# Kernel tuning notes

Measured on AMD Instinct MI355X. Metric: run time of the kernel, lower is better.

The kernel has to match this reference:

```python
import jax, jax.numpy as jnp
import numpy as np

NEG_INF = -1e10  # matches torch's -10000000000.0 fill


def setup_inputs() -> dict:
    key = jax.random.key(0)
    k1, k2, k3, k4, k5, k6 = jax.random.split(key, 6)
    B, N, D_IN, D_HID, D_OUT = 8, 2048, 512, 512, 512
    H = jax.random.normal(k1, (B, N, D_IN), dtype=jnp.float32)
    bias = jax.random.normal(k2, (B, N, N), dtype=jnp.float32)
    mask = jax.random.randint(k3, (B, N, N), 0, 2, dtype=jnp.int32)
    s = 1.0 / np.sqrt(D_IN)
    Wq = jax.random.normal(k4, (D_IN, D_HID), dtype=jnp.float32) * s
    Wk = jax.random.normal(k5, (D_IN, D_HID), dtype=jnp.float32) * s
    Wv = jax.random.normal(k6, (D_IN, D_OUT), dtype=jnp.float32) * s
    return {"H": H, "bias": bias, "mask": mask, "Wq": Wq, "Wk": Wk, "Wv": Wv}


def reference(H, bias, mask, Wq, Wk, Wv):
    # Q,K: [B,N,d_hid], V: [B,N,d_out]
    Q = H @ Wq
    K = H @ Wk
    V = H @ Wv
    d = Q.shape[-1]
    scale = 1.0 / jnp.sqrt(jnp.asarray(d, dtype=Q.dtype))
    # scores: [B,N,N]; scale, add bias, then fill masked-out entries
    scores = jnp.einsum("bnd,bmd->bnm", Q, K) * scale + bias
    scores = jnp.where(mask == 0, jnp.asarray(NEG_INF, scores.dtype), scores)
    atn = jax.nn.softmax(scores, axis=-1)
    return jnp.einsum("bnm,bmo->bno", atn, V)
```

## Files before the change

### kernel.cpp

```cpp
#include <hip/hip_runtime.h>
#include <hip/hip_bf16.h>

typedef __attribute__((ext_vector_type(8))) short short8;
typedef __attribute__((ext_vector_type(4))) float floatx4;
typedef __attribute__((ext_vector_type(4))) int intx4;
typedef __attribute__((ext_vector_type(4))) unsigned short ushortx4;

#define NB 8
#define NN 2048
#define DD 512

__device__ __forceinline__ unsigned short f2bf(float f) {
  union { float f; unsigned int u; } v; v.f = f;
  unsigned int u = v.u;
  return (unsigned short)((u + 0x7fffu + ((u >> 16) & 1u)) >> 16);
}
__device__ __forceinline__ float bf2f(unsigned short s) {
  union { unsigned int u; float f; } v; v.u = ((unsigned int)s) << 16;
  return v.f;
}

typedef __attribute__((address_space(3))) unsigned short lds_us;
typedef __attribute__((address_space(1))) const unsigned short glb_us;

__device__ __forceinline__ void ld_lds16(const unsigned short* g, unsigned short* l) {
  __builtin_amdgcn_global_load_lds((glb_us*)g, (lds_us*)l, 16, 0, 0);
}

__global__ __launch_bounds__(256) void mha_cvtH(const float* __restrict__ H,
                                                unsigned short* __restrict__ Hb, int n8) {
  int i = blockIdx.x * 256 + threadIdx.x;
  if (i >= n8) return;
  const float4* src = (const float4*)H;
  float4 a = src[2 * i], b = src[2 * i + 1];
  short8 o;
  o[0] = (short)f2bf(a.x); o[1] = (short)f2bf(a.y); o[2] = (short)f2bf(a.z); o[3] = (short)f2bf(a.w);
  o[4] = (short)f2bf(b.x); o[5] = (short)f2bf(b.y); o[6] = (short)f2bf(b.z); o[7] = (short)f2bf(b.w);
  *(short8*)(Hb + 8 * i) = o;
}

__global__ __launch_bounds__(256) void mha_prep(const floatx4* __restrict__ bias,
                                                const intx4* __restrict__ mask,
                                                ushortx4* __restrict__ bm) {
  int i = blockIdx.x * 256 + threadIdx.x;
  floatx4 bv = __builtin_nontemporal_load(&bias[i]);
  intx4 mv = __builtin_nontemporal_load(&mask[i]);
  const unsigned short NINF = 0xFF80;
  ushortx4 o;
  o.x = mv.x ? f2bf(bv.x) : NINF;
  o.y = mv.y ? f2bf(bv.y) : NINF;
  o.z = mv.z ? f2bf(bv.z) : NINF;
  o.w = mv.w ? f2bf(bv.w) : NINF;
  __builtin_nontemporal_store(o, &bm[i]);
}

__global__ __launch_bounds__(256) void mha_tW(const float* __restrict__ Wq, const float* __restrict__ Wk,
                                              const float* __restrict__ Wv,
                                              unsigned short* __restrict__ Wqt, unsigned short* __restrict__ Wkt,
                                              unsigned short* __restrict__ Wvt) {
  const float* W = (blockIdx.z == 0) ? Wq : (blockIdx.z == 1) ? Wk : Wv;
  unsigned short* Wt = (blockIdx.z == 0) ? Wqt : (blockIdx.z == 1) ? Wkt : Wvt;
  __shared__ float tile[32][33];
  int d0 = blockIdx.x * 32, k0 = blockIdx.y * 32;
  int t = threadIdx.x, r = t >> 3, c4 = (t & 7) * 4;
  float4 v = *(const float4*)(W + (size_t)(k0 + r) * DD + d0 + c4);
  tile[r][c4] = v.x; tile[r][c4 + 1] = v.y; tile[r][c4 + 2] = v.z; tile[r][c4 + 3] = v.w;
  __syncthreads();
  union { unsigned short s[4]; uint2 v; } u;
  u.s[0] = f2bf(tile[c4][r]);     u.s[1] = f2bf(tile[c4 + 1][r]);
  u.s[2] = f2bf(tile[c4 + 2][r]); u.s[3] = f2bf(tile[c4 + 3][r]);
  *(uint2*)(Wt + (size_t)(d0 + r) * DD + k0 + c4) = u.v;
}

__global__ __launch_bounds__(256) void mha_tV(const unsigned short* __restrict__ Vr,
                                              unsigned short* __restrict__ Vt) {
  int b = blockIdx.z;
  int d0 = blockIdx.x * 32, n0 = blockIdx.y * 32;
  __shared__ unsigned short tile[32][34];
  int t = threadIdx.x, r = t >> 3, c4 = (t & 7) * 4;
  union { uint2 v; unsigned short s[4]; } u;
  u.v = *(const uint2*)(Vr + ((size_t)b * NN + n0 + r) * DD + d0 + c4);
  tile[r][c4] = u.s[0]; tile[r][c4 + 1] = u.s[1]; tile[r][c4 + 2] = u.s[2]; tile[r][c4 + 3] = u.s[3];
  __syncthreads();
  union { unsigned short s[4]; uint2 v; } o;
  o.s[0] = tile[c4][r]; o.s[1] = tile[c4 + 1][r]; o.s[2] = tile[c4 + 2][r]; o.s[3] = tile[c4 + 3][r];
  *(uint2*)(Vt + ((size_t)b * DD + d0 + r) * NN + n0 + c4) = o.v;
}

__device__ __forceinline__ void stage_tile_async(const unsigned short* __restrict__ g, int ld,
                                                 unsigned short* s, int t) {
#pragma unroll
  for (int h = 0; h < 2; ++h) {
    int c = t + h * 256;
    int r = c >> 2, p = c & 3;
    int seg = (p - (r >> 1)) & 3;
    ld_lds16(g + (size_t)r * ld + seg * 8, s + c * 8);
  }
}

__device__ __forceinline__ void mfma_step(const unsigned short* As, const unsigned short* Bs,
                                          int wr, int wc, int quad, int lr, floatx4 acc[4][4]) {
  short8 a[4], b[4];
#pragma unroll
  for (int i = 0; i < 4; ++i) {
    int ra = wr * 64 + i * 16 + lr;
    int rb = wc * 64 + i * 16 + lr;
    a[i] = *(const short8*)(As + ra * 32 + ((quad + (ra >> 1)) & 3) * 8);
    b[i] = *(const short8*)(Bs + rb * 32 + ((quad + (rb >> 1)) & 3) * 8);
  }
#pragma unroll
  for (int i = 0; i < 4; ++i)
#pragma unroll
    for (int j = 0; j < 4; ++j)
      acc[i][j] = __builtin_amdgcn_mfma_f32_16x16x32_bf16(a[i], b[j], acc[i][j], 0, 0, 0);
}

__global__ __launch_bounds__(256) void mha_proj(const unsigned short* __restrict__ Hb,
                                                const unsigned short* __restrict__ Wqt,
                                                const unsigned short* __restrict__ Wkt,
                                                const unsigned short* __restrict__ Wvt,
                                                unsigned short* __restrict__ Qb,
                                                unsigned short* __restrict__ Kb,
                                                unsigned short* __restrict__ Vr) {
  const unsigned short* Wt = (blockIdx.z == 0) ? Wqt : (blockIdx.z == 1) ? Wkt : Wvt;
  unsigned short* dst = (blockIdx.z == 0) ? Qb : (blockIdx.z == 1) ? Kb : Vr;
  __shared__ unsigned short As[128 * 32], Bs[128 * 32];
  int t = threadIdx.x, wave = t >> 6, lane = t & 63, quad = lane >> 4, lr = lane & 15;
  int wr = wave >> 1, wc = wave & 1;
  int m0 = blockIdx.y * 128, n0 = blockIdx.x * 128;
  floatx4 acc[4][4] = {};
  for (int k0 = 0; k0 < DD; k0 += 32) {
    __syncthreads();
    stage_tile_async(Hb + (size_t)m0 * DD + k0, DD, As, t);
    stage_tile_async(Wt + (size_t)n0 * DD + k0, DD, Bs, t);
    __syncthreads();
    mfma_step(As, Bs, wr, wc, quad, lr, acc);
  }
#pragma unroll
  for (int i = 0; i < 4; ++i)
#pragma unroll
    for (int j = 0; j < 4; ++j)
#pragma unroll
      for (int r = 0; r < 4; ++r) {
        int row = m0 + wr * 64 + i * 16 + quad * 4 + r;
        int col = n0 + wc * 64 + j * 16 + lr;
        dst[(size_t)row * DD + col] = f2bf(acc[i][j][r]);
      }
}

__global__ __launch_bounds__(512) void mha_attn(const unsigned short* __restrict__ Qb,
                                                const unsigned short* __restrict__ Kb,
                                                const unsigned short* __restrict__ Vtb,
                                                const unsigned short* __restrict__ bmE,
                                                float* __restrict__ out) {
  __shared__ unsigned short KV[2][16384];
  __shared__ unsigned short Ps[64 * 128];
  __shared__ unsigned short Bm[64 * 128];
  __shared__ float ls[64];

  const int b = blockIdx.x;
  const int i0 = blockIdx.y * 64;
  const int t = threadIdx.x;
  const int wave = t >> 6, lane = t & 63, quad = lane >> 4, lr = lane & 15;
  const int wi = wave & 3;
  const int wj = wave >> 2;
  const float scale = 0.04419417382415922f;

  const unsigned short* Q = Qb + (size_t)b * NN * DD;
  const unsigned short* K = Kb + (size_t)b * NN * DD;
  const unsigned short* V = Vtb + (size_t)b * DD * NN;
  const unsigned short* bm = bmE + (size_t)b * NN * NN;

  if (t < 64) ls[t] = 0.0f;

  short8 q[16];
#pragma unroll
  for (int kc = 0; kc < 16; ++kc)
    q[kc] = *(const short8*)(Q + (size_t)(i0 + wi * 16 + lr) * DD + kc * 32 + quad * 8);

  floatx4 acc_o[4][4] = {};
  float rs[4] = {0.f, 0.f, 0.f, 0.f};

  const int krow = t >> 2, kphys = t & 3;
  const int kseg = (kphys - (krow >> 1)) & 3;

#pragma unroll
  for (int h = 0; h < 4; ++h)
    ld_lds16(K + (size_t)krow * DD + h * 32 + kseg * 8, KV[0] + h * 4096 + t * 8);
#pragma unroll
  for (int h = 0; h < 2; ++h) {
    int c = t + h * 512, row = c >> 4, phys = c & 15, seg = (phys - row) & 15;
    ld_lds16(bm + (size_t)(i0 + row) * NN + seg * 8, Bm + c * 8);
  }
  __syncthreads();

  for (int tt = 0; tt < 16; ++tt) {
    const int j0 = tt * 128;
    floatx4 acc_s[4] = {};

#pragma unroll
    for (int s = 0; s < 4; ++s) {
      if (s < 3) {
#pragma unroll
        for (int h = 0; h < 4; ++h)
          ld_lds16(K + (size_t)(j0 + krow) * DD + (s + 1) * 128 + h * 32 + kseg * 8,
                   KV[(s + 1) & 1] + h * 4096 + t * 8);
      } else {
#pragma unroll
        for (int h = 0; h < 4; ++h) {
          int c = t + h * 512, row = c >> 2, phys = c & 3, seg = (phys - (row >> 1)) & 3;
          ld_lds16(V + (size_t)row * NN + j0 + seg * 8, KV[0] + c * 8);
        }
      }
      const unsigned short* Ks = KV[s & 1];
#pragma unroll
      for (int kc = 0; kc < 4; ++kc) {
#pragma unroll
        for (int jt = 0; jt < 4; ++jt) {
          int rb = wj * 64 + jt * 16 + lr;
          short8 bf = *(const short8*)(Ks + kc * 4096 + rb * 32 + ((quad + (rb >> 1)) & 3) * 8);
          acc_s[jt] = __builtin_amdgcn_mfma_f32_16x16x32_bf16(q[s * 4 + kc], bf, acc_s[jt], 0, 0, 0);
        }
      }
      if (s == 3) {
#pragma unroll
        for (int jt = 0; jt < 4; ++jt) {
          int col = wj * 64 + jt * 16 + lr;
#pragma unroll
          for (int rr = 0; rr < 4; ++rr) {
            int row = wi * 16 + quad * 4 + rr;
            float bi = bf2f(Bm[row * 128 + ((((col >> 3) + row) & 15) << 3) + (col & 7)]);
            float e = __expf(acc_s[jt][rr] * scale + bi - 16.0f);
            unsigned short eb = f2bf(e);
            rs[rr] += bf2f(eb);
            Ps[row * 128 + (col ^ ((row & 7) << 3))] = eb;
          }
        }
      }
      __syncthreads();
    }

#pragma unroll
    for (int jc = 0; jc < 4; ++jc) {
      if (jc < 3) {
#pragma unroll
        for (int h = 0; h < 4; ++h) {
          int c = t + h * 512, row = c >> 2, phys = c & 3, seg = (phys - (row >> 1)) & 3;
          ld_lds16(V + (size_t)row * NN + j0 + (jc + 1) * 32 + seg * 8, KV[(jc + 1) & 1] + c * 8);
        }
      } else if (tt < 15) {
#pragma unroll
        for (int h = 0; h < 4; ++h)
          ld_lds16(K + (size_t)(j0 + 128 + krow) * DD + h * 32 + kseg * 8,
                   KV[0] + h * 4096 + t * 8);
#pragma unroll
        for (int h = 0; h < 2; ++h) {
          int c = t + h * 512, row = c >> 4, phys = c & 15, seg = (phys - row) & 15;
          ld_lds16(bm + (size_t)(i0 + row) * NN + j0 + 128 + seg * 8, Bm + c * 8);
        }
      }
      const unsigned short* Vs = KV[jc & 1];
      short8 pa[4];
#pragma unroll
      for (int it = 0; it < 4; ++it)
        pa[it] = *(const short8*)(Ps + (it * 16 + lr) * 128 +
                                  ((jc * 32 + quad * 8) ^ ((lr & 7) << 3)));
#pragma unroll
      for (int dt = 0; dt < 4; ++dt) {
        int rb = wave * 64 + dt * 16 + lr;
        short8 bf = *(const short8*)(Vs + rb * 32 + ((quad + (rb >> 1)) & 3) * 8);
#pragma unroll
        for (int it = 0; it < 4; ++it)
          acc_o[it][dt] = __builtin_amdgcn_mfma_f32_16x16x32_bf16(pa[it], bf, acc_o[it][dt], 0, 0, 0);
      }
      __syncthreads();
    }
  }

#pragma unroll
  for (int rr = 0; rr < 4; ++rr) {
    float v = rs[rr];
    v += __shfl_xor(v, 1);
    v += __shfl_xor(v, 2);
    v += __shfl_xor(v, 4);
    v += __shfl_xor(v, 8);
    if (lr == 0) atomicAdd(&ls[wi * 16 + quad * 4 + rr], v);
  }
  __syncthreads();

  float* ob = out + ((size_t)b * NN + i0) * DD;
#pragma unroll
  for (int it = 0; it < 4; ++it)
#pragma unroll
    for (int rr = 0; rr < 4; ++rr) {
      int row = it * 16 + quad * 4 + rr;
      float linv = 1.0f / ls[row];
#pragma unroll
      for (int dt = 0; dt < 4; ++dt)
        __builtin_nontemporal_store(acc_o[it][dt][rr] * linv,
                                    &ob[(size_t)row * DD + wave * 64 + dt * 16 + lr]);
    }
}

extern "C" void kernel_launch(void* const* d_in, const int* in_sizes, int n_in,
                              void* d_out, int out_size, void* d_ws, size_t ws_size,
                              hipStream_t stream) {
  const float* H = (const float*)d_in[0];
  const float* bias = (const float*)d_in[1];
  const int* mask = (const int*)d_in[2];
  const float* Wq = (const float*)d_in[3];
  const float* Wk = (const float*)d_in[4];
  const float* Wv = (const float*)d_in[5];
  float* out = (float*)d_out;
  char* ws = (char*)d_ws;

  const size_t SZ_QKV = (size_t)NB * NN * DD * 2;
  const size_t SZ_W = (size_t)DD * DD * 2;
  unsigned short* Qb = (unsigned short*)(ws);
  unsigned short* Kb = (unsigned short*)(ws + SZ_QKV);
  unsigned short* Vt = (unsigned short*)(ws + 2 * SZ_QKV);
  char* base2 = ws + 3 * SZ_QKV;
  unsigned short* bmE = (unsigned short*)(base2);
  unsigned short* Hb = (unsigned short*)(base2);
  unsigned short* Wqt = (unsigned short*)(base2 + SZ_QKV);
  unsigned short* Wkt = (unsigned short*)(base2 + SZ_QKV + SZ_W);
  unsigned short* Wvt = (unsigned short*)(base2 + SZ_QKV + 2 * SZ_W);
  unsigned short* Vr = (unsigned short*)(base2 + SZ_QKV + 3 * SZ_W);

  mha_cvtH<<<dim3((NB * NN * DD / 8) / 256), 256, 0, stream>>>(H, Hb, NB * NN * DD / 8);
  mha_tW<<<dim3(DD / 32, DD / 32, 3), 256, 0, stream>>>(Wq, Wk, Wv, Wqt, Wkt, Wvt);
  mha_proj<<<dim3(DD / 128, NB * NN / 128, 3), 256, 0, stream>>>(Hb, Wqt, Wkt, Wvt, Qb, Kb, Vr);
  mha_tV<<<dim3(DD / 32, NN / 32, NB), 256, 0, stream>>>(Vr, Vt);
  mha_prep<<<dim3((NB * NN * NN / 4) / 256), 256, 0, stream>>>((const floatx4*)bias,
                                                               (const intx4*)mask, (ushortx4*)bmE);
  mha_attn<<<dim3(NB, NN / 64), 512, 0, stream>>>(Qb, Kb, Vt, bmE, out);
}
```

Measured before the change: 471.8 us.

## Triple-buffer K/V LDS staging with fine-grained vmcnt waits and MFMA priority

Replaces the double-buffered K/V LDS ring, which was guarded by full __syncthreads, with a three-slot rotating buffer. Each stage now waits only on partial vmcnt counts followed by a bare s_barrier, so two global-to-LDS loads can stay in flight while MFMAs run. The MFMA loops are wrapped in s_setprio to favour compute issue, and the row-sum scratch reuses the Ps buffer to offset the extra LDS. The risks are added LDS per block (a third 32KB slot), which may lower occupancy, and correctness depending on hand-counted waitcnt values. The final iteration also prefetches a wrapped-around tile that is never used.

```diff
diff --git a/kernel.cpp b/kernel.cpp
--- a/kernel.cpp
+++ b/kernel.cpp
@@ -9,6 +9,11 @@
 #define NB 8
 #define NN 2048
 #define DD 512
+
+#define WAITV(N) asm volatile("s_waitcnt vmcnt(" #N ")" ::: "memory")
+#define WAITLK() asm volatile("s_waitcnt lgkmcnt(0)" ::: "memory")
+#define BAR() __builtin_amdgcn_s_barrier()
+#define CLOB() asm volatile("" ::: "memory")
 
 __device__ __forceinline__ unsigned short f2bf(float f) {
   union { float f; unsigned int u; } v; v.f = f;
@@ -148,15 +153,76 @@
       }
 }
 
+
+__device__ __forceinline__ void stageK(const unsigned short* __restrict__ K, int j0, int kblk,
+                                       unsigned short* buf, int krow, int kseg, int t) {
+#pragma unroll
+  for (int h = 0; h < 4; ++h)
+    ld_lds16(K + (size_t)(j0 + krow) * DD + kblk * 128 + h * 32 + kseg * 8,
+             buf + h * 4096 + t * 8);
+}
+
+__device__ __forceinline__ void stageV(const unsigned short* __restrict__ V, int j0, int jc,
+                                       unsigned short* buf, int t) {
+#pragma unroll
+  for (int h = 0; h < 4; ++h) {
+    int c = t + h * 512, row = c >> 2, phys = c & 3, seg = (phys - (row >> 1)) & 3;
+    ld_lds16(V + (size_t)row * NN + j0 + jc * 32 + seg * 8, buf + c * 8);
+  }
+}
+
+__device__ __forceinline__ void stageBm(const unsigned short* __restrict__ bm, int i0, int j0,
+                                        unsigned short* Bm, int t) {
+#pragma unroll
+  for (int h = 0; h < 2; ++h) {
+    int c = t + h * 512, row = c >> 4, phys = c & 15, seg = (phys - row) & 15;
+    ld_lds16(bm + (size_t)(i0 + row) * NN + j0 + seg * 8, Bm + c * 8);
+  }
+}
+
+template <int SQ>
+__device__ __forceinline__ void qk_stage(const unsigned short* Ks, const short8* q,
+                                         int wj, int quad, int lr, floatx4 (&acc_s)[4]) {
+  __builtin_amdgcn_s_setprio(1);
+#pragma unroll
+  for (int kc = 0; kc < 4; ++kc) {
+#pragma unroll
+    for (int jt = 0; jt < 4; ++jt) {
+      int rb = wj * 64 + jt * 16 + lr;
+      short8 bf = *(const short8*)(Ks + kc * 4096 + rb * 32 + ((quad + (rb >> 1)) & 3) * 8);
+      acc_s[jt] = __builtin_amdgcn_mfma_f32_16x16x32_bf16(q[SQ * 4 + kc], bf, acc_s[jt], 0, 0, 0);
+    }
+  }
+  __builtin_amdgcn_s_setprio(0);
+}
+
+template <int JC>
+__device__ __forceinline__ void pv_stage(const unsigned short* Vs, const unsigned short* Ps,
+                                         int wave, int quad, int lr, floatx4 (&acc_o)[4][4]) {
+  short8 pa[4];
+#pragma unroll
+  for (int it = 0; it < 4; ++it)
+    pa[it] = *(const short8*)(Ps + (it * 16 + lr) * 128 + ((JC * 32 + quad * 8) ^ ((lr & 7) << 3)));
+  __builtin_amdgcn_s_setprio(1);
+#pragma unroll
+  for (int dt = 0; dt < 4; ++dt) {
+    int rb = wave * 64 + dt * 16 + lr;
+    short8 bf = *(const short8*)(Vs + rb * 32 + ((quad + (rb >> 1)) & 3) * 8);
+#pragma unroll
+    for (int it = 0; it < 4; ++it)
+      acc_o[it][dt] = __builtin_amdgcn_mfma_f32_16x16x32_bf16(pa[it], bf, acc_o[it][dt], 0, 0, 0);
+  }
+  __builtin_amdgcn_s_setprio(0);
+}
+
 __global__ __launch_bounds__(512) void mha_attn(const unsigned short* __restrict__ Qb,
                                                 const unsigned short* __restrict__ Kb,
                                                 const unsigned short* __restrict__ Vtb,
                                                 const unsigned short* __restrict__ bmE,
                                                 float* __restrict__ out) {
-  __shared__ unsigned short KV[2][16384];
+  __shared__ unsigned short KV[3][16384];
   __shared__ unsigned short Ps[64 * 128];
   __shared__ unsigned short Bm[64 * 128];
-  __shared__ float ls[64];
 
   const int b = blockIdx.x;
   const int i0 = blockIdx.y * 64;
@@ -170,113 +236,102 @@
   const unsigned short* K = Kb + (size_t)b * NN * DD;
   const unsigned short* V = Vtb + (size_t)b * DD * NN;
   const unsigned short* bm = bmE + (size_t)b * NN * NN;
-
-  if (t < 64) ls[t] = 0.0f;
+  unsigned short* const KB = &KV[0][0];
+
+  const int krow = t >> 2, kphys = t & 3;
+  const int kseg = (kphys - (krow >> 1)) & 3;
 
   short8 q[16];
 #pragma unroll
   for (int kc = 0; kc < 16; ++kc)
     q[kc] = *(const short8*)(Q + (size_t)(i0 + wi * 16 + lr) * DD + kc * 32 + quad * 8);
+  CLOB();
 
   floatx4 acc_o[4][4] = {};
   float rs[4] = {0.f, 0.f, 0.f, 0.f};
 
-  const int krow = t >> 2, kphys = t & 3;
-  const int kseg = (kphys - (krow >> 1)) & 3;
-
-#pragma unroll
-  for (int h = 0; h < 4; ++h)
-    ld_lds16(K + (size_t)krow * DD + h * 32 + kseg * 8, KV[0] + h * 4096 + t * 8);
-#pragma unroll
-  for (int h = 0; h < 2; ++h) {
-    int c = t + h * 512, row = c >> 4, phys = c & 15, seg = (phys - row) & 15;
-    ld_lds16(bm + (size_t)(i0 + row) * NN + seg * 8, Bm + c * 8);
-  }
-  __syncthreads();
-
+  stageK(K, 0, 0, KB, krow, kseg, t);
+  stageK(K, 0, 1, KB + 16384, krow, kseg, t);
+  stageBm(bm, i0, 0, Bm, t);
+  CLOB();
+
+  int cb = 0;
   for (int tt = 0; tt < 16; ++tt) {
     const int j0 = tt * 128;
+    const int j0n = ((tt + 1) & 15) * 128;
     floatx4 acc_s[4] = {};
-
-#pragma unroll
-    for (int s = 0; s < 4; ++s) {
-      if (s < 3) {
-#pragma unroll
-        for (int h = 0; h < 4; ++h)
-          ld_lds16(K + (size_t)(j0 + krow) * DD + (s + 1) * 128 + h * 32 + kseg * 8,
-                   KV[(s + 1) & 1] + h * 4096 + t * 8);
-      } else {
-#pragma unroll
-        for (int h = 0; h < 4; ++h) {
-          int c = t + h * 512, row = c >> 2, phys = c & 3, seg = (phys - (row >> 1)) & 3;
-          ld_lds16(V + (size_t)row * NN + j0 + seg * 8, KV[0] + c * 8);
-        }
+    int ib;
+
+    WAITV(4); BAR();
+    ib = cb ? cb - 1 : 2;
+    stageK(K, j0, 2, KB + ib * 16384, krow, kseg, t); CLOB();
+    qk_stage<0>(KB + cb * 16384, q, wj, quad, lr, acc_s);
+    cb = (cb == 2) ? 0 : cb + 1;
+
+    WAITV(4); BAR();
+    ib = cb ? cb - 1 : 2;
+    stageK(K, j0, 3, KB + ib * 16384, krow, kseg, t); CLOB();
+    qk_stage<1>(KB + cb * 16384, q, wj, quad, lr, acc_s);
+    cb = (cb == 2) ? 0 : cb + 1;
+
+    WAITV(4); BAR();
+    ib = cb ? cb - 1 : 2;
+    stageV(V, j0, 0, KB + ib * 16384, t); CLOB();
+    qk_stage<2>(KB + cb * 16384, q, wj, quad, lr, acc_s);
+    cb = (cb == 2) ? 0 : cb + 1;
+
+    WAITV(4); BAR();
+    ib = cb ? cb - 1 : 2;
+    stageV(V, j0, 1, KB + ib * 16384, t); CLOB();
+    qk_stage<3>(KB + cb * 16384, q, wj, quad, lr, acc_s);
+    cb = (cb == 2) ? 0 : cb + 1;
+#pragma unroll
+    for (int jt = 0; jt < 4; ++jt) {
+      int col = wj * 64 + jt * 16 + lr;
+#pragma unroll
+      for (int rr = 0; rr < 4; ++rr) {
+        int row = wi * 16 + quad * 4 + rr;
+        float bi = bf2f(Bm[row * 128 + ((((col >> 3) + row) & 15) << 3) + (col & 7)]);
+        float sv = acc_s[jt][rr] * scale + bi - 16.0f;
+        float e = __expf(sv);
+        unsigned short eb = f2bf(e);
+        rs[rr] += bf2f(eb);
+        Ps[row * 128 + (col ^ ((row & 7) << 3))] = eb;
       }
-      const unsigned short* Ks = KV[s & 1];
-#pragma unroll
-      for (int kc = 0; kc < 4; ++kc) {
-#pragma unroll
-        for (int jt = 0; jt < 4; ++jt) {
-          int rb = wj * 64 + jt * 16 + lr;
-          short8 bf = *(const short8*)(Ks + kc * 4096 + rb * 32 + ((quad + (rb >> 1)) & 3) * 8);
-          acc_s[jt] = __builtin_amdgcn_mfma_f32_16x16x32_bf16(q[s * 4 + kc], bf, acc_s[jt], 0, 0, 0);
-        }
-      }
-      if (s == 3) {
-#pragma unroll
-        for (int jt = 0; jt < 4; ++jt) {
-          int col = wj * 64 + jt * 16 + lr;
-#pragma unroll
-          for (int rr = 0; rr < 4; ++rr) {
-            int row = wi * 16 + quad * 4 + rr;
-            float bi = bf2f(Bm[row * 128 + ((((col >> 3) + row) & 15) << 3) + (col & 7)]);
-            float e = __expf(acc_s[jt][rr] * scale + bi - 16.0f);
-            unsigned short eb = f2bf(e);
-            rs[rr] += bf2f(eb);
-            Ps[row * 128 + (col ^ ((row & 7) << 3))] = eb;
-          }
-        }
-      }
-      __syncthreads();
     }
 
-#pragma unroll
-    for (int jc = 0; jc < 4; ++jc) {
-      if (jc < 3) {
-#pragma unroll
-        for (int h = 0; h < 4; ++h) {
-          int c = t + h * 512, row = c >> 2, phys = c & 3, seg = (phys - (row >> 1)) & 3;
-          ld_lds16(V + (size_t)row * NN + j0 + (jc + 1) * 32 + seg * 8, KV[(jc + 1) & 1] + c * 8);
-        }
-      } else if (tt < 15) {
-#pragma unroll
-        for (int h = 0; h < 4; ++h)
-          ld_lds16(K + (size_t)(j0 + 128 + krow) * DD + h * 32 + kseg * 8,
-                   KV[0] + h * 4096 + t * 8);
-#pragma unroll
-        for (int h = 0; h < 2; ++h) {
-          int c = t + h * 512, row = c >> 4, phys = c & 15, seg = (phys - row) & 15;
-          ld_lds16(bm + (size_t)(i0 + row) * NN + j0 + 128 + seg * 8, Bm + c * 8);
-        }
-      }
-      const unsigned short* Vs = KV[jc & 1];
-      short8 pa[4];
-#pragma unroll
-      for (int it = 0; it < 4; ++it)
-        pa[it] = *(const short8*)(Ps + (it * 16 + lr) * 128 +
-                                  ((jc * 32 + quad * 8) ^ ((lr & 7) << 3)));
-#pragma unroll
-      for (int dt = 0; dt < 4; ++dt) {
-        int rb = wave * 64 + dt * 16 + lr;
-        short8 bf = *(const short8*)(Vs + rb * 32 + ((quad + (rb >> 1)) & 3) * 8);
-#pragma unroll
-        for (int it = 0; it < 4; ++it)
-          acc_o[it][dt] = __builtin_amdgcn_mfma_f32_16x16x32_bf16(pa[it], bf, acc_o[it][dt], 0, 0, 0);
-      }
-      __syncthreads();
-    }
-  }
-
+    WAITV(4); WAITLK(); BAR();
+    ib = cb ? cb - 1 : 2;
+    stageV(V, j0, 2, KB + ib * 16384, t);
+    stageBm(bm, i0, j0n, Bm, t);
+    CLOB();
+    pv_stage<0>(KB + cb * 16384, Ps, wave, quad, lr, acc_o);
+    cb = (cb == 2) ? 0 : cb + 1;
+
+    WAITV(6); BAR();
+    ib = cb ? cb - 1 : 2;
+    stageV(V, j0, 3, KB + ib * 16384, t); CLOB();
+    pv_stage<1>(KB + cb * 16384, Ps, wave, quad, lr, acc_o);
+    cb = (cb == 2) ? 0 : cb + 1;
+
+    WAITV(6); BAR();
+    ib = cb ? cb - 1 : 2;
+    stageK(K, j0n, 0, KB + ib * 16384, krow, kseg, t); CLOB();
+    pv_stage<2>(KB + cb * 16384, Ps, wave, quad, lr, acc_o);
+    cb = (cb == 2) ? 0 : cb + 1;
+
+    WAITV(4); BAR();
+    ib = cb ? cb - 1 : 2;
+    stageK(K, j0n, 1, KB + ib * 16384, krow, kseg, t); CLOB();
+    pv_stage<3>(KB + cb * 16384, Ps, wave, quad, lr, acc_o);
+    cb = (cb == 2) ? 0 : cb + 1;
+  }
+
+  __syncthreads();
+
+  float* lsf = (float*)Ps;
+  if (t < 64) lsf[t] = 0.0f;
+  __syncthreads();
 #pragma unroll
   for (int rr = 0; rr < 4; ++rr) {
     float v = rs[rr];
@@ -284,7 +339,7 @@
     v += __shfl_xor(v, 2);
     v += __shfl_xor(v, 4);
     v += __shfl_xor(v, 8);
-    if (lr == 0) atomicAdd(&ls[wi * 16 + quad * 4 + rr], v);
+    if (lr == 0) atomicAdd(&lsf[wi * 16 + quad * 4 + rr], v);
   }
   __syncthreads();
 
@@ -294,7 +349,7 @@
 #pragma unroll
     for (int rr = 0; rr < 4; ++rr) {
       int row = it * 16 + quad * 4 + rr;
-      float linv = 1.0f / ls[row];
+      float linv = 1.0f / lsf[row];
 #pragma unroll
       for (int dt = 0; dt < 4; ++dt)
         __builtin_nontemporal_store(acc_o[it][dt][rr] * linv,
```

After: 486.4 us. 1.03x slower.
